# Kernel tuning notes

Hardware: AMD Instinct MI355X
Metric: run time of the kernel (lower is better)

Reference implementation:

```python
import jax, jax.numpy as jnp
import numpy as np

# Config (mirrors CorrLayerDownsample(J=3, L=8, A=1, A_prime=1, M=256, N=256,
# num_channels=1, shift_mode='samec', mask_angles=4)). With samec + 1 channel,
# every pair is 'shifted' (mask index 1) and groups (j1,j2) are contiguous in
# the global moment order, so concatenation reproduces results_storage order.
J, L, A, M, N, NB = 3, 8, 1, 256, 256, 2
MASK_ANGLES = 4
RADII = (1, 2)  # dyadic shift radii (assumed form of create_masks_shift)

def _mask_positions():
    # shift mask 1: origin plus shifts along mask_angles directions at dyadic radii
    pos = {(0, 0)}
    for k in range(MASK_ANGLES):
        th = np.pi * k / MASK_ANGLES
        for r in RADII:
            pos.add((int(round(r * np.cos(th))), int(round(r * np.sin(th)))))
    return sorted(pos)

def _union_flat_idx(h, w):
    # row-major flat indices of the union shift mask at resolution (h, w),
    # matching torch boolean-mask indexing order (mask_downsample + mask_idx_map_1)
    return np.array(sorted(((dx % h) * w + (dy % w)) for dx, dy in _mask_positions()), dtype=np.int64)

UNION_IDX = [_union_flat_idx(M >> j, N >> j) for j in range(J)]
NSHIFT = len(UNION_IDX[0])

# per-(j1,j2) channel gather indices: la = A*L*c + A*l + a = l (A=1, c=0)
# loop order in compute_idx: l1 outer, l2 inner
LA1 = np.repeat(np.arange(L), L)
LA2 = np.tile(np.arange(L), L)

def _spectral_pad(xh, Mn, Nn):
    # zero-pad Fourier representation to (Mn, Nn) -- spectral upsampling
    m, n = xh.shape[-2], xh.shape[-1]
    if (m, n) == (Mn, Nn):
        return xh
    xs = jnp.fft.fftshift(xh, axes=(-2, -1))
    ph, pw = (Mn - m) // 2, (Nn - n) // 2
    pad = [(0, 0)] * (xh.ndim - 2) + [(ph, ph), (pw, pw)]
    xp = jnp.pad(xs, pad)
    return jnp.fft.ifftshift(xp, axes=(-2, -1)) * ((Mn * Nn) / (m * n))

def _forward(xpsi_0, xpsi_1, xpsi_2):
    xs = [xpsi_0, xpsi_1, xpsi_2]
    hats = [jnp.fft.fft2(x.astype(jnp.complex64)) for x in xs]  # [nb, C, h_j, w_j]
    la1 = jnp.asarray(LA1)
    la2 = jnp.asarray(LA2)
    outs = []
    for j1 in range(J):
        h, w = M >> j1, N >> j1
        uidx = jnp.asarray(UNION_IDX[j1])
        h1 = hats[j1][:, la1]  # [nb, P=L*L, h, w]
        for j2 in range(j1, J):
            h2 = hats[j2][:, la2]
            if j2 > j1:
                h2 = _spectral_pad(h2, h, w)  # upsample coarser scale to scale j1
            corr = jnp.fft.ifft2(h1 * jnp.conj(h2)).real  # cross-correlation map
            flat = corr.reshape(corr.shape[0], corr.shape[1], h * w)
            outs.append(flat[:, :, uidx])  # masked downsample: keep shift positions
    return jnp.concatenate(outs, axis=1)  # [nb, total_pairs, NSHIFT]

def setup_inputs():
    key = jax.random.key(0)
    ks = jax.random.split(key, 3)
    return {
        "xpsi_0": jax.random.normal(ks[0], (NB, A * L, M, N), dtype=jnp.float32),
        "xpsi_1": jax.random.normal(ks[1], (NB, A * L, M // 2, N // 2), dtype=jnp.float32),
        "xpsi_2": jax.random.normal(ks[2], (NB, A * L, M // 4, N // 4), dtype=jnp.float32),
    }

def reference(xpsi_0, xpsi_1, xpsi_2):
    return _forward(xpsi_0, xpsi_1, xpsi_2)
```

## Files before the change

kernel.cpp:

```cpp
#include <hip/hip_runtime.h>

#define PI_D 3.14159265358979323846
#define PI_F 3.14159265358979323846f


__device__ inline float rtab_val(int n, int m2, int t) {
  if (t == 0) return 1.0f;
  double th = PI_D * (double)t / (double)n;
  double v = sin(th * (double)(m2 - 1)) / sin(th) + cos(th * (double)m2);
  return (float)(v / (double)m2);
}

__global__ __launch_bounds__(256) void k_front(
    const float* __restrict__ X0, const float* __restrict__ X1,
    const float* __restrict__ X2, float* __restrict__ P1p,
    float* __restrict__ P2p, float* __restrict__ V01, float* __restrict__ V02,
    float* __restrict__ V12, float* __restrict__ T01, float* __restrict__ T02,
    float* __restrict__ T12, float* __restrict__ out) {
  __shared__ float fsm[2304];
  int bid = blockIdx.x;
  int t = threadIdx.x;
  if (bid == 512) {
    for (int i = t; i < 5376; i += 256) out[i] = 0.f;
    return;
  }
  if (bid < 192) {
    const float* X; float* P; int lg, nsp, idx0;
    if (bid < 128) { X = X1; P = P1p; lg = 7; nsp = 8; idx0 = bid; }
    else           { X = X2; P = P2p; lg = 6; nsp = 4; idx0 = bid - 128; }
    int ch = idx0 / nsp, split = idx0 % nsp;
    int n = 1 << lg;
    int total = n * n;
    int chunk = total / nsp;
    int b0 = split * chunk;
    const float* x = X + (size_t)ch * total + b0;
    float s = 0.f;
    for (int i = t; i < chunk; i += 256) {
      int idx = b0 + i;
      float v = x[i];
      s += (((idx >> lg) ^ idx) & 1) ? -v : v;
    }
#pragma unroll
    for (int off = 32; off > 0; off >>= 1) s += __shfl_down(s, off, 64);
    __shared__ float red[4];
    if ((t & 63) == 0) red[t >> 6] = s;
    __syncthreads();
    if (t == 0) P[ch * nsp + split] = red[0] + red[1] + red[2] + red[3];
    return;
  }
  if (bid < 320) {
    int idx = bid - 192;
    int ch = idx >> 3, nxg = (idx & 7) * 16;
    float* Rl = fsm;
    float* Xs = fsm + 256;
    for (int i = t; i < 256; i += 256) Rl[i] = rtab_val(256, 128, i);
    const float4* xch4 =
        (const float4*)(X1 + (size_t)ch * 16384 + (size_t)nxg * 128);
    for (int i = t; i < 512; i += 256) ((float4*)Xs)[i] = xch4[i];
    __syncthreads();
    if (idx == 0)
      for (int i = t; i < 256; i += 256) T01[i] = Rl[i];
    float* vch = V01 + (size_t)ch * 128 * 256;
    for (int i = t; i < 2048; i += 256) {
      int r = i >> 7, k = i & 127;
      vch[(size_t)(nxg + r) * 256 + 2 * k] = Xs[r * 128 + k];
    }
    int cid = t & 63, wq = t >> 6;
    int m0 = 2 * cid + 1, m1 = 2 * cid + 129;
    float acc[4][2];
#pragma unroll
    for (int r = 0; r < 4; ++r) { acc[r][0] = 0.f; acc[r][1] = 0.f; }
    for (int ny = 0; ny < 128; ++ny) {
      float r0 = Rl[(m0 - 2 * ny) & 255];
      float r1 = Rl[(m1 - 2 * ny) & 255];
#pragma unroll
      for (int r = 0; r < 4; ++r) {
        float xv = Xs[(4 * wq + r) * 128 + ny];
        acc[r][0] += xv * r0;
        acc[r][1] += xv * r1;
      }
    }
#pragma unroll
    for (int r = 0; r < 4; ++r) {
      vch[(size_t)(nxg + 4 * wq + r) * 256 + m0] = acc[r][0];
      vch[(size_t)(nxg + 4 * wq + r) * 256 + m1] = acc[r][1];
    }
    return;
  }
  {
    int vbid = bid - 320;
    const float* X = X2; float* V;
    int n1, n2, s, ch, nxg, colh;
    if (vbid < 128) {
      V = V02; n1 = 256; n2 = 64; s = 4;
      ch = vbid >> 3; nxg = ((vbid >> 1) & 3) * 16; colh = vbid & 1;
    } else {
      int w = vbid - 128;
      V = V12; n1 = 128; n2 = 64; s = 2;
      ch = w >> 2; nxg = (w & 3) * 16; colh = 0;
    }
    float* Rl = fsm;
    float* Xs = fsm + 256;
    for (int i = t; i < n1; i += 256) Rl[i] = rtab_val(n1, n2, i);
    const float4* xch4 =
        (const float4*)(X + (size_t)ch * n2 * n2 + (size_t)nxg * n2);
    int nx4 = (16 * n2) >> 2;
    for (int i = t; i < nx4; i += 256) ((float4*)Xs)[i] = xch4[i];
    __syncthreads();
    if (vbid == 0)
      for (int i = t; i < 256; i += 256) T02[i] = Rl[i];
    if (vbid == 128)
      for (int i = t; i < 128; i += 256) T12[i] = Rl[i];
    int myq = (t & 63) + colh * 128;
    int nxq = t >> 6;
    int mask = n1 - 1;
    float acc[4][2];
#pragma unroll
    for (int r = 0; r < 4; ++r)
#pragma unroll
      for (int c = 0; c < 2; ++c) acc[r][c] = 0.f;
    for (int ny = 0; ny < n2; ++ny) {
      float xv[4];
#pragma unroll
      for (int r = 0; r < 4; ++r) xv[r] = Xs[(4 * nxq + r) * n2 + ny];
#pragma unroll
      for (int c = 0; c < 2; ++c) {
        float rv = Rl[(myq + 64 * c - s * ny) & mask];
#pragma unroll
        for (int r = 0; r < 4; ++r) acc[r][c] += xv[r] * rv;
      }
    }
    float* vch = V + (size_t)ch * n2 * n1;
#pragma unroll
    for (int r = 0; r < 4; ++r)
      for (int c = 0; c < 2; ++c)
        vch[(size_t)(nxg + 4 * nxq + r) * n1 + myq + 64 * c] = acc[r][c];
  }
}

__global__ __launch_bounds__(256) void k_main(const float* __restrict__ X0,
                                              const float* __restrict__ X1,
                                              const float* __restrict__ X2,
                                              const float* __restrict__ V01,
                                              const float* __restrict__ V02,
                                              const float* __restrict__ V12,
                                              const float* __restrict__ P1p,
                                              const float* __restrict__ P2p,
                                              const float* __restrict__ T01,
                                              const float* __restrict__ T02,
                                              const float* __restrict__ T12,
                                              float* __restrict__ out) {
  __shared__ float sRl[256];
  __shared__ float sh[4864];
  __shared__ float Vs[2][1024];
  int u = blockIdx.x;
  int t = threadIdx.x;
  int lane = t & 63;
  int wv = t >> 6;

  int b, l2, base, lgn1, mxg;
  const float* A1b;

  if (u < 640) {
    const float* V; const float* Pp; const float* T;
    int n1, n2, s, ch, chunk, nsp; float inv;
    if (u < 256) {
      V = V01; Pp = P1p; nsp = 8; A1b = X0; n1 = 256; n2 = 128; s = 2;
      inv = 1.f / 16384.f; ch = u >> 4; chunk = u & 15; lgn1 = 8; base = 64;
      T = T01;
    } else if (u < 512) {
      int w = u - 256;
      V = V02; Pp = P2p; nsp = 4; A1b = X0; n1 = 256; n2 = 64; s = 4;
      inv = 1.f / 4096.f; ch = w >> 4; chunk = w & 15; lgn1 = 8; base = 128;
      T = T02;
    } else {
      int w = u - 512;
      V = V12; Pp = P2p; nsp = 4; A1b = X1; n1 = 128; n2 = 64; s = 2;
      inv = 1.f / 4096.f; ch = w >> 3; chunk = w & 7; lgn1 = 7; base = 256;
      T = T12;
    }
    int mask = n1 - 1;
    for (int i = t; i < n1; i += 256) sRl[i] = T[i];
    mxg = chunk * 16;
    b = ch >> 3; l2 = ch & 7;
    const float* vch = V + (size_t)ch * n2 * n1;
    float Pv = 0.f;
    for (int i = 0; i < nsp; ++i) Pv += Pp[ch * nsp + i];
    float a = PI_F / (float)s;
    int per = 2 * s;

    if (n1 == 256) {
      if (s == 2) {
        for (int i = t; i < 640; i += 256) {
          int rl = 2 * (i >> 6), c4 = (i & 63) * 4;
          int mx = (mxg - 2 + rl) & 255;
          *(float4*)&sh[rl * 256 + c4] =
              *(const float4*)(vch + (size_t)(mx >> 1) * 256 + c4);
        }
      } else {
        for (int i = t; i < 320; i += 256) {
          int rl = 2 + 4 * (i >> 6), c4 = (i & 63) * 4;
          int mx = (mxg - 2 + rl) & 255;
          *(float4*)&sh[rl * 256 + c4] =
              *(const float4*)(vch + (size_t)(mx >> 2) * 256 + c4);
        }
      }
    } else {
      for (int i = t; i < 320; i += 256) {
        int rl = 2 * (i >> 5), c4 = (i & 31) * 4;
        int mx = (mxg - 2 + rl) & 127;
        *(float4*)&sh[rl * 128 + c4] =
            *(const float4*)(vch + (size_t)(mx >> 1) * 128 + c4);
      }
    }

    int nr, rls[4];
    if (s == 2) {
      if (wv == 0)      { nr = 3; rls[0] = 1;  rls[1] = 3;  rls[2] = 5;  rls[3] = 1; }
      else if (wv == 1) { nr = 2; rls[0] = 7;  rls[1] = 9;  rls[2] = 7;  rls[3] = 7; }
      else if (wv == 2) { nr = 2; rls[0] = 11; rls[1] = 13; rls[2] = 11; rls[3] = 11; }
      else              { nr = 2; rls[0] = 15; rls[1] = 17; rls[2] = 15; rls[3] = 15; }
    } else {
      if (wv == 0)      { nr = 4; rls[0] = 0;  rls[1] = 1;  rls[2] = 3;  rls[3] = 4; }
      else if (wv == 1) { nr = 4; rls[0] = 5;  rls[1] = 7;  rls[2] = 8;  rls[3] = 9; }
      else if (wv == 2) { nr = 3; rls[0] = 11; rls[1] = 12; rls[2] = 13; rls[3] = 11; }
      else              { nr = 3; rls[0] = 15; rls[1] = 16; rls[2] = 17; rls[3] = 15; }
    }
    int bj[4];
#pragma unroll
    for (int j = 0; j < 4; ++j) bj[j] = (mxg - 2 + rls[j]) & mask;

    const float4* vp4 = (const float4*)vch;
    if (n1 == 256) {
      int ntl = n2 >> 2;
      ((float4*)Vs[0])[t] = vp4[t];
      __syncthreads();
      float4 acc[4];
#pragma unroll
      for (int j = 0; j < 4; ++j) acc[j] = make_float4(0.f, 0.f, 0.f, 0.f);
      for (int tl = 0; tl < ntl; ++tl) {
        float4 stg;
        bool has = (tl + 1 < ntl);
        if (has) stg = vp4[(size_t)(tl + 1) * 256 + t];
        const float* Vc = Vs[tl & 1];
#pragma unroll
        for (int kk = 0; kk < 4; ++kk) {
          float4 vv = *(const float4*)&Vc[kk * 256 + 4 * lane];
          int ss = s * (4 * tl + kk);
#pragma unroll
          for (int j = 0; j < 4; ++j)
            if (j < nr) {
              float rv = sRl[(bj[j] - ss) & 255];
              acc[j].x += rv * vv.x;
              acc[j].y += rv * vv.y;
              acc[j].z += rv * vv.z;
              acc[j].w += rv * vv.w;
            }
        }
        if (has) ((float4*)Vs[(tl & 1) ^ 1])[t] = stg;
        __syncthreads();
      }
      float smy[4];
#pragma unroll
      for (int j = 0; j < 4; ++j)
        smy[j] = sinf(a * (float)((4 * lane + j) & (per - 1)));
#pragma unroll
      for (int j = 0; j < 4; ++j)
        if (j < nr) {
          float q = inv * sinf(a * (float)(bj[j] & (per - 1))) * Pv;
          float4 o = acc[j];
          o.x -= q * smy[0];
          o.y -= q * smy[1];
          o.z -= q * smy[2];
          o.w -= q * smy[3];
          *(float4*)&sh[rls[j] * 256 + 4 * lane] = o;
        }
    } else {
      if (t < 128) ((float4*)Vs[0])[t] = vp4[t];
      __syncthreads();
      float2 acc[4];
#pragma unroll
      for (int j = 0; j < 4; ++j) acc[j] = make_float2(0.f, 0.f);
      for (int tl = 0; tl < 16; ++tl) {
        float4 stg;
        bool has = (tl + 1 < 16) && (t < 128);
        if (has) stg = vp4[(size_t)(tl + 1) * 128 + t];
        const float* Vc = Vs[tl & 1];
#pragma unroll
        for (int kk = 0; kk < 4; ++kk) {
          float2 vv = *(const float2*)&Vc[kk * 128 + 2 * lane];
          int ss = 2 * (4 * tl + kk);
#pragma unroll
          for (int j = 0; j < 4; ++j)
            if (j < nr) {
              float rv = sRl[(bj[j] - ss) & 127];
              acc[j].x += rv * vv.x;
              acc[j].y += rv * vv.y;
            }
        }
        if (has) ((float4*)Vs[(tl & 1) ^ 1])[t] = stg;
        __syncthreads();
      }
      const float a2 = PI_F * 0.5f;
      float smy0 = sinf(a2 * (float)((2 * lane) & 3));
      float smy1 = sinf(a2 * (float)((2 * lane + 1) & 3));
#pragma unroll
      for (int j = 0; j < 4; ++j)
        if (j < nr) {
          float q = inv * sinf(a2 * (float)(bj[j] & 3)) * Pv;
          float2 o = acc[j];
          o.x -= q * smy0;
          o.y -= q * smy1;
          *(float2*)&sh[rls[j] * 128 + 2 * lane] = o;
        }
    }
  } else {
    int w = u - 640;
    const float* Ab; int loc, lgc;
    if (w < 256)      { loc = w;       Ab = X0; lgn1 = 8; lgc = 4; base = 0;   }
    else if (w < 384) { loc = w - 256; Ab = X1; lgn1 = 7; lgc = 3; base = 192; }
    else              { loc = w - 384; Ab = X2; lgn1 = 6; lgc = 2; base = 320; }
    int n1 = 1 << lgn1;
    int mask = n1 - 1;
    int n1sq = n1 * n1;
    int chunk = loc & ((1 << lgc) - 1);
    int bl2 = loc >> lgc;
    b = bl2 >> 3; l2 = bl2 & 7;
    A1b = Ab;
    const float* A2 = Ab + (size_t)(b * 8 + l2) * n1sq;
    mxg = chunk * 16;
    int nst = (19 * n1) >> 2;
    int l2n1 = lgn1 - 2;
    for (int i = t; i < nst; i += 256) {
      int rl = i >> l2n1;
      int c4 = (i & ((n1 >> 2) - 1)) * 4;
      int src = (mxg - 2 + rl) & mask;
      *(float4*)&sh[rl * n1 + c4] = *(const float4*)(A2 + (size_t)src * n1 + c4);
    }
  }
  __syncthreads();

  float accC[8][7];
#pragma unroll
  for (int i = 0; i < 8; ++i)
#pragma unroll
    for (int p = 0; p < 7; ++p) accC[i][p] = 0.f;
  {
    int n1 = 1 << lgn1;
    int mask = n1 - 1;
    int n1sq = n1 * n1;
    int lgtpr = lgn1 - 2;
    int tpr = 1 << lgtpr;
    int rif = 256 >> lgtpr;
    int rid = t >> lgtpr;
    int cid2 = t & (tpr - 1);
    int ty = cid2 * 4;
    int tym = (ty - 4) & mask;
    const float* A1 = A1b + (size_t)(b * 8) * n1sq;
    for (int rr = 0; rr < 16; rr += rif) {
      int ri = rr + rid;
      const float* r0 = &sh[(ri + 2) * n1];
      const float* r1 = &sh[(ri + 1) * n1];
      const float* r2 = &sh[ri * n1];
      const float* r3 = &sh[(ri + 3) * n1];
      float4 a0 = *(const float4*)(r0 + tym);
      float4 b0 = *(const float4*)(r0 + ty);
      float4 a1 = *(const float4*)(r1 + tym);
      float4 b1 = *(const float4*)(r1 + ty);
      float4 b2 = *(const float4*)(r2 + ty);
      float4 a3 = *(const float4*)(r3 + tym);
      float4 b3 = *(const float4*)(r3 + ty);
      const float* rA = A1 + (size_t)(mxg + ri) * n1 + ty;
#pragma unroll
      for (int l1 = 0; l1 < 8; ++l1) {
        float4 xv = *(const float4*)(rA + (size_t)l1 * n1sq);
        accC[l1][0] += xv.x * b0.x + xv.y * b0.y + xv.z * b0.z + xv.w * b0.w;
        accC[l1][1] += xv.x * a0.w + xv.y * b0.x + xv.z * b0.y + xv.w * b0.z;
        accC[l1][2] += xv.x * a0.z + xv.y * a0.w + xv.z * b0.x + xv.w * b0.y;
        accC[l1][3] += xv.x * b1.x + xv.y * b1.y + xv.z * b1.z + xv.w * b1.w;
        accC[l1][4] += xv.x * a1.w + xv.y * b1.x + xv.z * b1.y + xv.w * b1.z;
        accC[l1][5] += xv.x * b2.x + xv.y * b2.y + xv.z * b2.z + xv.w * b2.w;
        accC[l1][6] += xv.x * a3.w + xv.y * b3.x + xv.z * b3.y + xv.w * b3.z;
      }
    }
  }

  float* af = &accC[0][0];
#pragma unroll
  for (int j = 0; j < 56; ++j) {
    float v = af[j];
    v += __shfl_down(v, 32, 64);
    v += __shfl_down(v, 16, 64);
    af[j] = v;
  }
  __syncthreads();
  if (lane < 16) {
    float* rowp = sh + (wv * 16 + lane) * 60;
#pragma unroll
    for (int j = 0; j < 14; ++j)
      *(float4*)&rowp[4 * j] =
          make_float4(af[4 * j], af[4 * j + 1], af[4 * j + 2], af[4 * j + 3]);
  }
  __syncthreads();
  if (t < 224) {
    int v = t >> 2, q = t & 3;
    float s2 = 0.f;
#pragma unroll
    for (int i = 0; i < 16; ++i) s2 += sh[(q * 16 + i) * 60 + v];
    s2 += __shfl_down(s2, 2, 64);
    s2 += __shfl_down(s2, 1, 64);
    if (q == 0) {
      int l1o = v / 7, p = v % 7;
      atomicAdd(&out[((size_t)b * 384 + base + l1o * 8 + l2) * 7 + p], s2);
    }
  }
}

extern "C" void kernel_launch(void* const* d_in, const int* in_sizes, int n_in,
                              void* d_out, int out_size, void* d_ws, size_t ws_size,
                              hipStream_t stream) {
  const float* X0 = (const float*)d_in[0];
  const float* X1 = (const float*)d_in[1];
  const float* X2 = (const float*)d_in[2];
  float* out = (float*)d_out;
  float* ws = (float*)d_ws;

  float* V01 = ws + 2359296;
  float* V02 = ws + 2883584;
  float* V12 = ws + 3145728;
  float* P1p = ws + 3276800;
  float* P2p = ws + 3276928;
  float* T01 = ws + 3276992;
  float* T02 = ws + 3277248;
  float* T12 = ws + 3277504;

  k_front<<<513, 256, 0, stream>>>(X0, X1, X2, P1p, P2p, V01, V02, V12, T01,
                                   T02, T12, out);
  k_main<<<1088, 256, 0, stream>>>(X0, X1, X2, V01, V02, V12, P1p, P2p, T01,
                                   T02, T12, out);
}
```

Baseline: 94.93 us.

## Triple-buffer V tile staging and interleave block-to-channel mapping

The main kernel's V-tile loop moves from a double buffer with one-tile-ahead prefetch to a triple-buffered LDS ring with two register-staged tiles in flight, unrolled by two. The aim is to hide global load latency behind more compute. Block indices in both kernels are also remapped so consecutive blocks walk across channels rather than chunks within one channel, which changes cache and memory-channel access patterns. The cost is more LDS use and more registers, which may lower occupancy.

```diff
diff --git a/kernel.cpp b/kernel.cpp
--- a/kernel.cpp
+++ b/kernel.cpp
@@ -10,6 +10,7 @@
   double v = sin(th * (double)(m2 - 1)) / sin(th) + cos(th * (double)m2);
   return (float)(v / (double)m2);
 }
+
 
 __global__ __launch_bounds__(256) void k_front(
     const float* __restrict__ X0, const float* __restrict__ X1,
@@ -50,7 +51,8 @@
   }
   if (bid < 320) {
     int idx = bid - 192;
-    int ch = idx >> 3, nxg = (idx & 7) * 16;
+    int ch = (idx & 7) + 8 * (idx >> 6);
+    int nxg = ((idx >> 3) & 7) * 16;
     float* Rl = fsm;
     float* Xs = fsm + 256;
     for (int i = t; i < 256; i += 256) Rl[i] = rtab_val(256, 128, i);
@@ -93,11 +95,14 @@
     int n1, n2, s, ch, nxg, colh;
     if (vbid < 128) {
       V = V02; n1 = 256; n2 = 64; s = 4;
-      ch = vbid >> 3; nxg = ((vbid >> 1) & 3) * 16; colh = vbid & 1;
+      ch = (vbid & 7) + 8 * (vbid >> 6);
+      int sub = (vbid >> 3) & 7;
+      nxg = ((sub >> 1) & 3) * 16; colh = sub & 1;
     } else {
       int w = vbid - 128;
       V = V12; n1 = 128; n2 = 64; s = 2;
-      ch = w >> 2; nxg = (w & 3) * 16; colh = 0;
+      ch = (w & 7) + 8 * (w >> 5);
+      nxg = ((w >> 3) & 3) * 16; colh = 0;
     }
     float* Rl = fsm;
     float* Xs = fsm + 256;
@@ -152,7 +157,7 @@
                                               float* __restrict__ out) {
   __shared__ float sRl[256];
   __shared__ float sh[4864];
-  __shared__ float Vs[2][1024];
+  __shared__ float VsB[3072];
   int u = blockIdx.x;
   int t = threadIdx.x;
   int lane = t & 63;
@@ -166,18 +171,21 @@
     int n1, n2, s, ch, chunk, nsp; float inv;
     if (u < 256) {
       V = V01; Pp = P1p; nsp = 8; A1b = X0; n1 = 256; n2 = 128; s = 2;
-      inv = 1.f / 16384.f; ch = u >> 4; chunk = u & 15; lgn1 = 8; base = 64;
-      T = T01;
+      inv = 1.f / 16384.f; lgn1 = 8; base = 64; T = T01;
+      ch = (u & 7) + 8 * (u >> 7);
+      chunk = (u >> 3) & 15;
     } else if (u < 512) {
       int w = u - 256;
       V = V02; Pp = P2p; nsp = 4; A1b = X0; n1 = 256; n2 = 64; s = 4;
-      inv = 1.f / 4096.f; ch = w >> 4; chunk = w & 15; lgn1 = 8; base = 128;
-      T = T02;
+      inv = 1.f / 4096.f; lgn1 = 8; base = 128; T = T02;
+      ch = (w & 7) + 8 * (w >> 7);
+      chunk = (w >> 3) & 15;
     } else {
       int w = u - 512;
       V = V12; Pp = P2p; nsp = 4; A1b = X1; n1 = 128; n2 = 64; s = 2;
-      inv = 1.f / 4096.f; ch = w >> 3; chunk = w & 7; lgn1 = 7; base = 256;
-      T = T12;
+      inv = 1.f / 4096.f; lgn1 = 7; base = 256; T = T12;
+      ch = (w & 7) + 8 * (w >> 6);
+      chunk = (w >> 3) & 7;
     }
     int mask = n1 - 1;
     for (int i = t; i < n1; i += 256) sRl[i] = T[i];
@@ -233,32 +241,59 @@
     const float4* vp4 = (const float4*)vch;
     if (n1 == 256) {
       int ntl = n2 >> 2;
-      ((float4*)Vs[0])[t] = vp4[t];
+      float* bc = VsB;
+      float* bn = VsB + 1024;
+      float* bo = VsB + 2048;
+      ((float4*)bc)[t] = vp4[t];
+      float4 rA = vp4[256 + t];
+      float4 rB = vp4[512 + t];
       __syncthreads();
       float4 acc[4];
 #pragma unroll
       for (int j = 0; j < 4; ++j) acc[j] = make_float4(0.f, 0.f, 0.f, 0.f);
-      for (int tl = 0; tl < ntl; ++tl) {
-        float4 stg;
-        bool has = (tl + 1 < ntl);
-        if (has) stg = vp4[(size_t)(tl + 1) * 256 + t];
-        const float* Vc = Vs[tl & 1];
-#pragma unroll
-        for (int kk = 0; kk < 4; ++kk) {
-          float4 vv = *(const float4*)&Vc[kk * 256 + 4 * lane];
-          int ss = s * (4 * tl + kk);
-#pragma unroll
-          for (int j = 0; j < 4; ++j)
-            if (j < nr) {
-              float rv = sRl[(bj[j] - ss) & 255];
-              acc[j].x += rv * vv.x;
-              acc[j].y += rv * vv.y;
-              acc[j].z += rv * vv.z;
-              acc[j].w += rv * vv.w;
-            }
-        }
-        if (has) ((float4*)Vs[(tl & 1) ^ 1])[t] = stg;
-        __syncthreads();
+      for (int tl = 0; tl < ntl; tl += 2) {
+        {
+          const float* Vc = bc;
+#pragma unroll
+          for (int kk = 0; kk < 4; ++kk) {
+            float4 vv = *(const float4*)&Vc[kk * 256 + 4 * lane];
+            int ss = s * (4 * tl + kk);
+#pragma unroll
+            for (int j = 0; j < 4; ++j)
+              if (j < nr) {
+                float rv = sRl[(bj[j] - ss) & 255];
+                acc[j].x += rv * vv.x;
+                acc[j].y += rv * vv.y;
+                acc[j].z += rv * vv.z;
+                acc[j].w += rv * vv.w;
+              }
+          }
+          if (tl + 1 < ntl) ((float4*)bn)[t] = rA;
+          if (tl + 3 < ntl) rA = vp4[(size_t)(tl + 3) * 256 + t];
+          __syncthreads();
+          float* tmp = bc; bc = bn; bn = bo; bo = tmp;
+        }
+        {
+          const float* Vc = bc;
+#pragma unroll
+          for (int kk = 0; kk < 4; ++kk) {
+            float4 vv = *(const float4*)&Vc[kk * 256 + 4 * lane];
+            int ss = s * (4 * (tl + 1) + kk);
+#pragma unroll
+            for (int j = 0; j < 4; ++j)
+              if (j < nr) {
+                float rv = sRl[(bj[j] - ss) & 255];
+                acc[j].x += rv * vv.x;
+                acc[j].y += rv * vv.y;
+                acc[j].z += rv * vv.z;
+                acc[j].w += rv * vv.w;
+              }
+          }
+          if (tl + 2 < ntl) ((float4*)bn)[t] = rB;
+          if (tl + 4 < ntl) rB = vp4[(size_t)(tl + 4) * 256 + t];
+          __syncthreads();
+          float* tmp = bc; bc = bn; bn = bo; bo = tmp;
+        }
       }
       float smy[4];
 #pragma unroll
@@ -276,30 +311,62 @@
           *(float4*)&sh[rls[j] * 256 + 4 * lane] = o;
         }
     } else {
-      if (t < 128) ((float4*)Vs[0])[t] = vp4[t];
+      float* bc = VsB;
+      float* bn = VsB + 512;
+      float* bo = VsB + 1024;
+      float4 rA, rB;
+      if (t < 128) {
+        ((float4*)bc)[t] = vp4[t];
+        rA = vp4[128 + t];
+        rB = vp4[256 + t];
+      }
       __syncthreads();
       float2 acc[4];
 #pragma unroll
       for (int j = 0; j < 4; ++j) acc[j] = make_float2(0.f, 0.f);
-      for (int tl = 0; tl < 16; ++tl) {
-        float4 stg;
-        bool has = (tl + 1 < 16) && (t < 128);
-        if (has) stg = vp4[(size_t)(tl + 1) * 128 + t];
-        const float* Vc = Vs[tl & 1];
-#pragma unroll
-        for (int kk = 0; kk < 4; ++kk) {
-          float2 vv = *(const float2*)&Vc[kk * 128 + 2 * lane];
-          int ss = 2 * (4 * tl + kk);
-#pragma unroll
-          for (int j = 0; j < 4; ++j)
-            if (j < nr) {
-              float rv = sRl[(bj[j] - ss) & 127];
-              acc[j].x += rv * vv.x;
-              acc[j].y += rv * vv.y;
-            }
-        }
-        if (has) ((float4*)Vs[(tl & 1) ^ 1])[t] = stg;
-        __syncthreads();
+      for (int tl = 0; tl < 16; tl += 2) {
+        {
+          const float* Vc = bc;
+#pragma unroll
+          for (int kk = 0; kk < 4; ++kk) {
+            float2 vv = *(const float2*)&Vc[kk * 128 + 2 * lane];
+            int ss = 2 * (4 * tl + kk);
+#pragma unroll
+            for (int j = 0; j < 4; ++j)
+              if (j < nr) {
+                float rv = sRl[(bj[j] - ss) & 127];
+                acc[j].x += rv * vv.x;
+                acc[j].y += rv * vv.y;
+              }
+          }
+          if (t < 128) {
+            if (tl + 1 < 16) ((float4*)bn)[t] = rA;
+            if (tl + 3 < 16) rA = vp4[(size_t)(tl + 3) * 128 + t];
+          }
+          __syncthreads();
+          float* tmp = bc; bc = bn; bn = bo; bo = tmp;
+        }
+        {
+          const float* Vc = bc;
+#pragma unroll
+          for (int kk = 0; kk < 4; ++kk) {
+            float2 vv = *(const float2*)&Vc[kk * 128 + 2 * lane];
+            int ss = 2 * (4 * (tl + 1) + kk);
+#pragma unroll
+            for (int j = 0; j < 4; ++j)
+              if (j < nr) {
+                float rv = sRl[(bj[j] - ss) & 127];
+                acc[j].x += rv * vv.x;
+                acc[j].y += rv * vv.y;
+              }
+          }
+          if (t < 128) {
+            if (tl + 2 < 16) ((float4*)bn)[t] = rB;
+            if (tl + 4 < 16) rB = vp4[(size_t)(tl + 4) * 128 + t];
+          }
+          __syncthreads();
+          float* tmp = bc; bc = bn; bn = bo; bo = tmp;
+        }
       }
       const float a2 = PI_F * 0.5f;
       float smy0 = sinf(a2 * (float)((2 * lane) & 3));
```

Result: no change. 95.34 us, median of 2 (+0.4%).

## Split upsampling into separate kernel materializing full-resolution upsampled planes

Applied to the files above, without the earlier changes.

The row-direction spectral upsampling was previously recomputed inside each k_main block for its 16-row chunk plus halo rows. It now moves into a new k_up kernel that writes full upsampled planes U01/U02/U12 to workspace once. k_main then loads these planes the same way it loads the native-scale inputs, which removes the redundant halo recomputation and simplifies its prologue. The cost is an extra kernel launch and extra global memory traffic to write and re-read the upsampled planes. k_front's block-to-channel mapping is also reordered.

```diff
diff --git a/kernel.cpp b/kernel.cpp
--- a/kernel.cpp
+++ b/kernel.cpp
@@ -12,18 +12,13 @@
 }
 
 __global__ __launch_bounds__(256) void k_front(
-    const float* __restrict__ X0, const float* __restrict__ X1,
-    const float* __restrict__ X2, float* __restrict__ P1p,
-    float* __restrict__ P2p, float* __restrict__ V01, float* __restrict__ V02,
-    float* __restrict__ V12, float* __restrict__ T01, float* __restrict__ T02,
-    float* __restrict__ T12, float* __restrict__ out) {
+    const float* __restrict__ X1, const float* __restrict__ X2,
+    float* __restrict__ P1p, float* __restrict__ P2p, float* __restrict__ V01,
+    float* __restrict__ V02, float* __restrict__ V12, float* __restrict__ T01,
+    float* __restrict__ T02, float* __restrict__ T12) {
   __shared__ float fsm[2304];
   int bid = blockIdx.x;
   int t = threadIdx.x;
-  if (bid == 512) {
-    for (int i = t; i < 5376; i += 256) out[i] = 0.f;
-    return;
-  }
   if (bid < 192) {
     const float* X; float* P; int lg, nsp, idx0;
     if (bid < 128) { X = X1; P = P1p; lg = 7; nsp = 8; idx0 = bid; }
@@ -50,7 +45,8 @@
   }
   if (bid < 320) {
     int idx = bid - 192;
-    int ch = idx >> 3, nxg = (idx & 7) * 16;
+    int ch = (idx & 7) + 8 * (idx >> 6);
+    int nxg = ((idx >> 3) & 7) * 16;
     float* Rl = fsm;
     float* Xs = fsm + 256;
     for (int i = t; i < 256; i += 256) Rl[i] = rtab_val(256, 128, i);
@@ -93,11 +89,14 @@
     int n1, n2, s, ch, nxg, colh;
     if (vbid < 128) {
       V = V02; n1 = 256; n2 = 64; s = 4;
-      ch = vbid >> 3; nxg = ((vbid >> 1) & 3) * 16; colh = vbid & 1;
+      ch = (vbid & 7) + 8 * (vbid >> 6);
+      int sub = (vbid >> 3) & 7;
+      nxg = ((sub >> 1) & 3) * 16; colh = sub & 1;
     } else {
       int w = vbid - 128;
       V = V12; n1 = 128; n2 = 64; s = 2;
-      ch = w >> 2; nxg = (w & 3) * 16; colh = 0;
+      ch = (w & 7) + 8 * (w >> 5);
+      nxg = ((w >> 3) & 3) * 16; colh = 0;
     }
     float* Rl = fsm;
     float* Xs = fsm + 256;
@@ -138,205 +137,228 @@
   }
 }
 
+__global__ __launch_bounds__(256) void k_up(
+    const float* __restrict__ V01, const float* __restrict__ V02,
+    const float* __restrict__ V12, const float* __restrict__ P1p,
+    const float* __restrict__ P2p, const float* __restrict__ T01,
+    const float* __restrict__ T02, const float* __restrict__ T12,
+    float* __restrict__ U01, float* __restrict__ U02,
+    float* __restrict__ U12, float* __restrict__ out) {
+  __shared__ float sRl[256];
+  __shared__ float Vt[2][2048];
+  int bid = blockIdx.x;
+  int t = threadIdx.x;
+  int lane = t & 63, wv = t >> 6;
+  if (bid == 640) {
+    for (int i = t; i < 5376; i += 256) out[i] = 0.f;
+    return;
+  }
+  const float* V; const float* Pp; const float* T; float* U;
+  int n1, n2, s, ch, grp, nsp; float inv;
+  if (bid < 256) {
+    V = V01; Pp = P1p; T = T01; U = U01; nsp = 8;
+    n1 = 256; n2 = 128; s = 2; inv = 1.f / 16384.f;
+    ch = bid >> 4; grp = bid & 15;
+  } else if (bid < 512) {
+    int w = bid - 256;
+    V = V02; Pp = P2p; T = T02; U = U02; nsp = 4;
+    n1 = 256; n2 = 64; s = 4; inv = 1.f / 4096.f;
+    ch = w >> 4; grp = w & 15;
+  } else {
+    int w = bid - 512;
+    V = V12; Pp = P2p; T = T12; U = U12; nsp = 4;
+    n1 = 128; n2 = 64; s = 2; inv = 1.f / 4096.f;
+    ch = w >> 3; grp = w & 7;
+  }
+  for (int i = t; i < n1; i += 256) sRl[i] = T[i];
+  const float* vch = V + (size_t)ch * n2 * n1;
+  float* uch = U + (size_t)ch * n1 * n1;
+  float Pv = 0.f;
+  for (int i = 0; i < nsp; ++i) Pv += Pp[ch * nsp + i];
+  float a = PI_F / (float)s;
+  int per = 2 * s;
+  int r0g = grp * 16;
+  const float4* vp4 = (const float4*)vch;
+
+  if (n1 == 256) {
+    if (s == 2) {
+      for (int i = t; i < 512; i += 256) {
+        int k = i >> 6, c4 = (i & 63) * 4;
+        int mx = r0g + 2 * k;
+        *(float4*)&uch[(size_t)mx * 256 + c4] =
+            *(const float4*)(vch + (size_t)(mx >> 1) * 256 + c4);
+      }
+    } else {
+      for (int i = t; i < 256; i += 256) {
+        int k = i >> 6, c4 = (i & 63) * 4;
+        int mx = r0g + 4 * k;
+        *(float4*)&uch[(size_t)mx * 256 + c4] =
+            *(const float4*)(vch + (size_t)(mx >> 2) * 256 + c4);
+      }
+    }
+    int nr = (s == 2) ? 2 : 3;
+    int bj0 = r0g + 4 * wv + 1;
+    int bj1 = r0g + 4 * wv + ((s == 2) ? 3 : 2);
+    int bj2 = r0g + 4 * wv + 3;
+    float4 acc0 = make_float4(0.f, 0.f, 0.f, 0.f);
+    float4 acc1 = make_float4(0.f, 0.f, 0.f, 0.f);
+    float4 acc2 = make_float4(0.f, 0.f, 0.f, 0.f);
+    int ntl = n2 >> 3;
+    for (int i = t; i < 512; i += 256) ((float4*)Vt[0])[i] = vp4[i];
+    __syncthreads();
+    for (int tl = 0; tl < ntl; ++tl) {
+      float4 stg0, stg1;
+      bool has = (tl + 1 < ntl);
+      if (has) {
+        stg0 = vp4[(size_t)(tl + 1) * 512 + t];
+        stg1 = vp4[(size_t)(tl + 1) * 512 + 256 + t];
+      }
+      const float* Vc = Vt[tl & 1];
+#pragma unroll
+      for (int kk = 0; kk < 8; ++kk) {
+        float4 vv = *(const float4*)&Vc[kk * 256 + 4 * lane];
+        int ss = s * (8 * tl + kk);
+        float r0v = sRl[(bj0 - ss) & 255];
+        float r1v = sRl[(bj1 - ss) & 255];
+        acc0.x += r0v * vv.x; acc0.y += r0v * vv.y;
+        acc0.z += r0v * vv.z; acc0.w += r0v * vv.w;
+        acc1.x += r1v * vv.x; acc1.y += r1v * vv.y;
+        acc1.z += r1v * vv.z; acc1.w += r1v * vv.w;
+        if (nr == 3) {
+          float r2v = sRl[(bj2 - ss) & 255];
+          acc2.x += r2v * vv.x; acc2.y += r2v * vv.y;
+          acc2.z += r2v * vv.z; acc2.w += r2v * vv.w;
+        }
+      }
+      if (has) {
+        float4* d = (float4*)Vt[(tl & 1) ^ 1];
+        d[t] = stg0;
+        d[256 + t] = stg1;
+      }
+      __syncthreads();
+    }
+    float smy[4];
+#pragma unroll
+    for (int j = 0; j < 4; ++j)
+      smy[j] = sinf(a * (float)((4 * lane + j) & (per - 1)));
+    {
+      float q = inv * sinf(a * (float)(bj0 & (per - 1))) * Pv;
+      float4 o = acc0;
+      o.x -= q * smy[0]; o.y -= q * smy[1]; o.z -= q * smy[2]; o.w -= q * smy[3];
+      *(float4*)&uch[(size_t)bj0 * 256 + 4 * lane] = o;
+    }
+    {
+      float q = inv * sinf(a * (float)(bj1 & (per - 1))) * Pv;
+      float4 o = acc1;
+      o.x -= q * smy[0]; o.y -= q * smy[1]; o.z -= q * smy[2]; o.w -= q * smy[3];
+      *(float4*)&uch[(size_t)bj1 * 256 + 4 * lane] = o;
+    }
+    if (nr == 3) {
+      float q = inv * sinf(a * (float)(bj2 & (per - 1))) * Pv;
+      float4 o = acc2;
+      o.x -= q * smy[0]; o.y -= q * smy[1]; o.z -= q * smy[2]; o.w -= q * smy[3];
+      *(float4*)&uch[(size_t)bj2 * 256 + 4 * lane] = o;
+    }
+  } else {
+    for (int i = t; i < 256; i += 256) {
+      int k = i >> 5, c4 = (i & 31) * 4;
+      int mx = r0g + 2 * k;
+      *(float4*)&uch[(size_t)mx * 128 + c4] =
+          *(const float4*)(vch + (size_t)(mx >> 1) * 128 + c4);
+    }
+    int bj0 = r0g + 4 * wv + 1;
+    int bj1 = r0g + 4 * wv + 3;
+    float2 acc0 = make_float2(0.f, 0.f);
+    float2 acc1 = make_float2(0.f, 0.f);
+    for (int i = t; i < 256; i += 256) ((float4*)Vt[0])[i] = vp4[i];
+    __syncthreads();
+    for (int tl = 0; tl < 8; ++tl) {
+      float4 stg0;
+      bool has = (tl + 1 < 8);
+      if (has) stg0 = vp4[(size_t)(tl + 1) * 256 + t];
+      const float* Vc = Vt[tl & 1];
+#pragma unroll
+      for (int kk = 0; kk < 8; ++kk) {
+        float2 vv = *(const float2*)&Vc[kk * 128 + 2 * lane];
+        int ss = 2 * (8 * tl + kk);
+        float r0v = sRl[(bj0 - ss) & 127];
+        float r1v = sRl[(bj1 - ss) & 127];
+        acc0.x += r0v * vv.x; acc0.y += r0v * vv.y;
+        acc1.x += r1v * vv.x; acc1.y += r1v * vv.y;
+      }
+      if (has) ((float4*)Vt[(tl & 1) ^ 1])[t] = stg0;
+      __syncthreads();
+    }
+    const float a2 = PI_F * 0.5f;
+    float smy0 = sinf(a2 * (float)((2 * lane) & 3));
+    float smy1 = sinf(a2 * (float)((2 * lane + 1) & 3));
+    {
+      float q = inv * sinf(a2 * (float)(bj0 & 3)) * Pv;
+      float2 o = acc0; o.x -= q * smy0; o.y -= q * smy1;
+      *(float2*)&uch[(size_t)bj0 * 128 + 2 * lane] = o;
+    }
+    {
+      float q = inv * sinf(a2 * (float)(bj1 & 3)) * Pv;
+      float2 o = acc1; o.x -= q * smy0; o.y -= q * smy1;
+      *(float2*)&uch[(size_t)bj1 * 128 + 2 * lane] = o;
+    }
+  }
+}
+
 __global__ __launch_bounds__(256) void k_main(const float* __restrict__ X0,
                                               const float* __restrict__ X1,
                                               const float* __restrict__ X2,
-                                              const float* __restrict__ V01,
-                                              const float* __restrict__ V02,
-                                              const float* __restrict__ V12,
-                                              const float* __restrict__ P1p,
-                                              const float* __restrict__ P2p,
-                                              const float* __restrict__ T01,
-                                              const float* __restrict__ T02,
-                                              const float* __restrict__ T12,
+                                              const float* __restrict__ U01,
+                                              const float* __restrict__ U02,
+                                              const float* __restrict__ U12,
                                               float* __restrict__ out) {
-  __shared__ float sRl[256];
   __shared__ float sh[4864];
-  __shared__ float Vs[2][1024];
   int u = blockIdx.x;
   int t = threadIdx.x;
-  int lane = t & 63;
-  int wv = t >> 6;
-
+  int lane = t & 63, wv = t >> 6;
+  const float* A1b; const float* S;
   int b, l2, base, lgn1, mxg;
-  const float* A1b;
-
   if (u < 640) {
-    const float* V; const float* Pp; const float* T;
-    int n1, n2, s, ch, chunk, nsp; float inv;
+    int ch, chunk;
     if (u < 256) {
-      V = V01; Pp = P1p; nsp = 8; A1b = X0; n1 = 256; n2 = 128; s = 2;
-      inv = 1.f / 16384.f; ch = u >> 4; chunk = u & 15; lgn1 = 8; base = 64;
-      T = T01;
+      A1b = X0; lgn1 = 8; base = 64;
+      ch = u >> 4; chunk = u & 15;
+      S = U01 + (size_t)ch * 65536;
     } else if (u < 512) {
       int w = u - 256;
-      V = V02; Pp = P2p; nsp = 4; A1b = X0; n1 = 256; n2 = 64; s = 4;
-      inv = 1.f / 4096.f; ch = w >> 4; chunk = w & 15; lgn1 = 8; base = 128;
-      T = T02;
+      A1b = X0; lgn1 = 8; base = 128;
+      ch = w >> 4; chunk = w & 15;
+      S = U02 + (size_t)ch * 65536;
     } else {
       int w = u - 512;
-      V = V12; Pp = P2p; nsp = 4; A1b = X1; n1 = 128; n2 = 64; s = 2;
-      inv = 1.f / 4096.f; ch = w >> 3; chunk = w & 7; lgn1 = 7; base = 256;
-      T = T12;
-    }
-    int mask = n1 - 1;
-    for (int i = t; i < n1; i += 256) sRl[i] = T[i];
-    mxg = chunk * 16;
-    b = ch >> 3; l2 = ch & 7;
-    const float* vch = V + (size_t)ch * n2 * n1;
-    float Pv = 0.f;
-    for (int i = 0; i < nsp; ++i) Pv += Pp[ch * nsp + i];
-    float a = PI_F / (float)s;
-    int per = 2 * s;
-
-    if (n1 == 256) {
-      if (s == 2) {
-        for (int i = t; i < 640; i += 256) {
-          int rl = 2 * (i >> 6), c4 = (i & 63) * 4;
-          int mx = (mxg - 2 + rl) & 255;
-          *(float4*)&sh[rl * 256 + c4] =
-              *(const float4*)(vch + (size_t)(mx >> 1) * 256 + c4);
-        }
-      } else {
-        for (int i = t; i < 320; i += 256) {
-          int rl = 2 + 4 * (i >> 6), c4 = (i & 63) * 4;
-          int mx = (mxg - 2 + rl) & 255;
-          *(float4*)&sh[rl * 256 + c4] =
-              *(const float4*)(vch + (size_t)(mx >> 2) * 256 + c4);
-        }
-      }
-    } else {
-      for (int i = t; i < 320; i += 256) {
-        int rl = 2 * (i >> 5), c4 = (i & 31) * 4;
-        int mx = (mxg - 2 + rl) & 127;
-        *(float4*)&sh[rl * 128 + c4] =
-            *(const float4*)(vch + (size_t)(mx >> 1) * 128 + c4);
-      }
-    }
-
-    int nr, rls[4];
-    if (s == 2) {
-      if (wv == 0)      { nr = 3; rls[0] = 1;  rls[1] = 3;  rls[2] = 5;  rls[3] = 1; }
-      else if (wv == 1) { nr = 2; rls[0] = 7;  rls[1] = 9;  rls[2] = 7;  rls[3] = 7; }
-      else if (wv == 2) { nr = 2; rls[0] = 11; rls[1] = 13; rls[2] = 11; rls[3] = 11; }
-      else              { nr = 2; rls[0] = 15; rls[1] = 17; rls[2] = 15; rls[3] = 15; }
-    } else {
-      if (wv == 0)      { nr = 4; rls[0] = 0;  rls[1] = 1;  rls[2] = 3;  rls[3] = 4; }
-      else if (wv == 1) { nr = 4; rls[0] = 5;  rls[1] = 7;  rls[2] = 8;  rls[3] = 9; }
-      else if (wv == 2) { nr = 3; rls[0] = 11; rls[1] = 12; rls[2] = 13; rls[3] = 11; }
-      else              { nr = 3; rls[0] = 15; rls[1] = 16; rls[2] = 17; rls[3] = 15; }
-    }
-    int bj[4];
-#pragma unroll
-    for (int j = 0; j < 4; ++j) bj[j] = (mxg - 2 + rls[j]) & mask;
-
-    const float4* vp4 = (const float4*)vch;
-    if (n1 == 256) {
-      int ntl = n2 >> 2;
-      ((float4*)Vs[0])[t] = vp4[t];
-      __syncthreads();
-      float4 acc[4];
-#pragma unroll
-      for (int j = 0; j < 4; ++j) acc[j] = make_float4(0.f, 0.f, 0.f, 0.f);
-      for (int tl = 0; tl < ntl; ++tl) {
-        float4 stg;
-        bool has = (tl + 1 < ntl);
-        if (has) stg = vp4[(size_t)(tl + 1) * 256 + t];
-        const float* Vc = Vs[tl & 1];
-#pragma unroll
-        for (int kk = 0; kk < 4; ++kk) {
-          float4 vv = *(const float4*)&Vc[kk * 256 + 4 * lane];
-          int ss = s * (4 * tl + kk);
-#pragma unroll
-          for (int j = 0; j < 4; ++j)
-            if (j < nr) {
-              float rv = sRl[(bj[j] - ss) & 255];
-              acc[j].x += rv * vv.x;
-              acc[j].y += rv * vv.y;
-              acc[j].z += rv * vv.z;
-              acc[j].w += rv * vv.w;
-            }
-        }
-        if (has) ((float4*)Vs[(tl & 1) ^ 1])[t] = stg;
-        __syncthreads();
-      }
-      float smy[4];
-#pragma unroll
-      for (int j = 0; j < 4; ++j)
-        smy[j] = sinf(a * (float)((4 * lane + j) & (per - 1)));
-#pragma unroll
-      for (int j = 0; j < 4; ++j)
-        if (j < nr) {
-          float q = inv * sinf(a * (float)(bj[j] & (per - 1))) * Pv;
-          float4 o = acc[j];
-          o.x -= q * smy[0];
-          o.y -= q * smy[1];
-          o.z -= q * smy[2];
-          o.w -= q * smy[3];
-          *(float4*)&sh[rls[j] * 256 + 4 * lane] = o;
-        }
-    } else {
-      if (t < 128) ((float4*)Vs[0])[t] = vp4[t];
-      __syncthreads();
-      float2 acc[4];
-#pragma unroll
-      for (int j = 0; j < 4; ++j) acc[j] = make_float2(0.f, 0.f);
-      for (int tl = 0; tl < 16; ++tl) {
-        float4 stg;
-        bool has = (tl + 1 < 16) && (t < 128);
-        if (has) stg = vp4[(size_t)(tl + 1) * 128 + t];
-        const float* Vc = Vs[tl & 1];
-#pragma unroll
-        for (int kk = 0; kk < 4; ++kk) {
-          float2 vv = *(const float2*)&Vc[kk * 128 + 2 * lane];
-          int ss = 2 * (4 * tl + kk);
-#pragma unroll
-          for (int j = 0; j < 4; ++j)
-            if (j < nr) {
-              float rv = sRl[(bj[j] - ss) & 127];
-              acc[j].x += rv * vv.x;
-              acc[j].y += rv * vv.y;
-            }
-        }
-        if (has) ((float4*)Vs[(tl & 1) ^ 1])[t] = stg;
-        __syncthreads();
-      }
-      const float a2 = PI_F * 0.5f;
-      float smy0 = sinf(a2 * (float)((2 * lane) & 3));
-      float smy1 = sinf(a2 * (float)((2 * lane + 1) & 3));
-#pragma unroll
-      for (int j = 0; j < 4; ++j)
-        if (j < nr) {
-          float q = inv * sinf(a2 * (float)(bj[j] & 3)) * Pv;
-          float2 o = acc[j];
-          o.x -= q * smy0;
-          o.y -= q * smy1;
-          *(float2*)&sh[rls[j] * 128 + 2 * lane] = o;
-        }
-    }
+      A1b = X1; lgn1 = 7; base = 256;
+      ch = w >> 3; chunk = w & 7;
+      S = U12 + (size_t)ch * 16384;
+    }
+    b = ch >> 3; l2 = ch & 7; mxg = chunk * 16;
   } else {
     int w = u - 640;
     const float* Ab; int loc, lgc;
     if (w < 256)      { loc = w;       Ab = X0; lgn1 = 8; lgc = 4; base = 0;   }
     else if (w < 384) { loc = w - 256; Ab = X1; lgn1 = 7; lgc = 3; base = 192; }
     else              { loc = w - 384; Ab = X2; lgn1 = 6; lgc = 2; base = 320; }
-    int n1 = 1 << lgn1;
-    int mask = n1 - 1;
-    int n1sq = n1 * n1;
+    int n1sq = 1 << (2 * lgn1);
     int chunk = loc & ((1 << lgc) - 1);
     int bl2 = loc >> lgc;
     b = bl2 >> 3; l2 = bl2 & 7;
     A1b = Ab;
-    const float* A2 = Ab + (size_t)(b * 8 + l2) * n1sq;
+    S = Ab + (size_t)(b * 8 + l2) * n1sq;
     mxg = chunk * 16;
-    int nst = (19 * n1) >> 2;
-    int l2n1 = lgn1 - 2;
-    for (int i = t; i < nst; i += 256) {
-      int rl = i >> l2n1;
-      int c4 = (i & ((n1 >> 2) - 1)) * 4;
-      int src = (mxg - 2 + rl) & mask;
-      *(float4*)&sh[rl * n1 + c4] = *(const float4*)(A2 + (size_t)src * n1 + c4);
-    }
+  }
+  int n1 = 1 << lgn1, mask = n1 - 1;
+
+  int nst = (19 * n1) >> 2;
+  int l2n1 = lgn1 - 2;
+  for (int i = t; i < nst; i += 256) {
+    int rl = i >> l2n1;
+    int c4 = (i & ((n1 >> 2) - 1)) * 4;
+    int src = (mxg - 2 + rl) & mask;
+    *(float4*)&sh[rl * n1 + c4] = *(const float4*)(S + (size_t)src * n1 + c4);
   }
   __syncthreads();
 
@@ -346,8 +368,6 @@
 #pragma unroll
     for (int p = 0; p < 7; ++p) accC[i][p] = 0.f;
   {
-    int n1 = 1 << lgn1;
-    int mask = n1 - 1;
     int n1sq = n1 * n1;
     int lgtpr = lgn1 - 2;
     int tpr = 1 << lgtpr;
@@ -425,6 +445,9 @@
   float* out = (float*)d_out;
   float* ws = (float*)d_ws;
 
+  float* U01 = ws;
+  float* U02 = ws + 1048576;
+  float* U12 = ws + 2097152;
   float* V01 = ws + 2359296;
   float* V02 = ws + 2883584;
   float* V12 = ws + 3145728;
@@ -434,8 +457,9 @@
   float* T02 = ws + 3277248;
   float* T12 = ws + 3277504;
 
-  k_front<<<513, 256, 0, stream>>>(X0, X1, X2, P1p, P2p, V01, V02, V12, T01,
-                                   T02, T12, out);
-  k_main<<<1088, 256, 0, stream>>>(X0, X1, X2, V01, V02, V12, P1p, P2p, T01,
-                                   T02, T12, out);
+  k_front<<<512, 256, 0, stream>>>(X1, X2, P1p, P2p, V01, V02, V12, T01, T02,
+                                   T12);
+  k_up<<<641, 256, 0, stream>>>(V01, V02, V12, P1p, P2p, T01, T02, T12, U01,
+                                U02, U12, out);
+  k_main<<<1088, 256, 0, stream>>>(X0, X1, X2, U01, U02, U12, out);
 }
```

Result: slower. 112.7 us (+18.7%).
